# Performance work log

Measured on AMD Instinct MI355X. Metric: run time of the kernel, lower is better.

The kernel has to match this reference:

```python
import jax, jax.numpy as jnp
import numpy as np

HIDDEN = 128

def setup_inputs() -> dict:
    key = jax.random.key(0)
    k1, k2, k3, k4, k5, k6 = jax.random.split(key, 6)
    n_nodes, n_edges, h = 100000, 500000, HIDDEN
    node_features_after_gcn = jax.random.normal(k1, (n_nodes, h), dtype=jnp.float32)
    edges = jax.random.randint(k2, (2, n_edges), 0, n_nodes, dtype=jnp.int64)
    # edge_classifier params: Linear(2h -> 4h), Linear(4h -> 2)
    W1 = jax.random.normal(k3, (2 * h, 4 * h), dtype=jnp.float32) / np.sqrt(2 * h)
    b1 = jax.random.normal(k4, (4 * h,), dtype=jnp.float32) * 0.01
    W2 = jax.random.normal(k5, (4 * h, 2), dtype=jnp.float32) / np.sqrt(4 * h)
    b2 = jax.random.normal(k6, (2,), dtype=jnp.float32) * 0.01
    return {"node_features_after_gcn": node_features_after_gcn, "edges": edges,
            "W1": W1, "b1": b1, "W2": W2, "b2": b2}

def reference(node_features_after_gcn, W1, b1, W2, b2, edges):
    # gather endpoint features: [E, h] each (node1/node2 projections are Identity)
    first = node_features_after_gcn[edges[0], :]
    second = node_features_after_gcn[edges[1], :]
    edge_feat = jnp.concatenate((first, second), axis=1)  # [E, 2h]
    edge_feat = jax.nn.relu(edge_feat)
    hidden = jax.nn.relu(edge_feat @ W1 + b1)  # [E, 4h]
    return hidden @ W2 + b2  # [E, 2]
```

## Files before the change

kernel.cpp:

```cpp
#include <hip/hip_runtime.h>
#include <stdint.h>

#define HID  128
#define N1   512
#define NCAT 1024
#define NTB  48

typedef _Float16 f16;
typedef __attribute__((ext_vector_type(8))) _Float16 f16x8;
typedef __attribute__((ext_vector_type(4))) _Float16 f16x4;
typedef __attribute__((ext_vector_type(8))) short   short8;
typedef __attribute__((ext_vector_type(4))) float   floatx4;
typedef __attribute__((ext_vector_type(2))) float   floatx2;
typedef __attribute__((ext_vector_type(8))) __bf16  bf16x8;

static __device__ __forceinline__ short f2bf(float x) {
  uint32_t u = __builtin_bit_cast(uint32_t, x);
  uint32_t r = (u + 0x7FFFu + ((u >> 16) & 1u)) >> 16;
  return (short)r;
}
static __device__ __forceinline__ float bf2f(short s) {
  uint32_t u = ((uint32_t)(uint16_t)s) << 16;
  return __builtin_bit_cast(float, u);
}

static __device__ __forceinline__ void gload16(const f16* g, f16* l) {
  __builtin_amdgcn_global_load_lds(
      (const __attribute__((address_space(1))) unsigned int*)g,
      (__attribute__((address_space(3))) unsigned int*)l, 16, 0, 0);
}


__global__ __launch_bounds__(256) void prep_all(
    const float* __restrict__ feats, const float* __restrict__ W1,
    f16* __restrict__ A, f16* __restrict__ BT2, int total4) {
  int idx = blockIdx.x * 256 + threadIdx.x;
  if (idx < total4) {
    floatx4 f = *(const floatx4*)(feats + (size_t)idx * 4);
    f16x4 o;
#pragma unroll
    for (int j = 0; j < 4; ++j) o[j] = (f16)fmaxf(f[j], 0.f);
    *(f16x4*)(A + (size_t)idx * 4) = o;
    return;
  }
  int w = idx - total4;
  if (w < N1 * 256) {
    int n = w >> 8;
    int k = w & 255;
    BT2[w] = (f16)W1[k * N1 + n];
  }
}

__global__ __launch_bounds__(512, 2) void fused_kernel(
    const f16* __restrict__ A,
    const f16* __restrict__ BT2,
    const float* __restrict__ b1,
    const float* __restrict__ W2,
    const float* __restrict__ b2,
    const int* __restrict__ edges,
    float* __restrict__ out,
    int n_edges, int ntiles) {
  __shared__ f16 AU[2][NTB][HID];
  __shared__ f16 AV[2][NTB][HID];
  __shared__ float   part[8][NTB][2];
  __shared__ float   b1s[N1];
  __shared__ floatx2 w2s[N1];

  const int tid  = threadIdx.x;
  const int wave = tid >> 6;
  const int lane = tid & 63;
  const int quad = lane >> 4;
  const int l16  = lane & 15;
  const int n0w  = wave << 6;

  if (tid < N1) {
    b1s[tid] = b1[tid];
    w2s[tid] = *(const floatx2*)(W2 + 2 * tid);
  }

  f16x8 bfr[4][8];
#pragma unroll
  for (int nn = 0; nn < 4; ++nn) {
    const f16* bp = BT2 + (size_t)(n0w + nn * 16 + l16) * 256 + quad * 8;
#pragma unroll
    for (int kk = 0; kk < 8; ++kk) bfr[nn][kk] = *(const f16x8*)(bp + kk * 32);
  }

  const int j0   = wave * 3;
  const int rsub = lane >> 4;

  int idr[3];
  auto load_idx = [&](int t) {
#pragma unroll
    for (int c = 0; c < 3; ++c) {
      int j = j0 + c;
      int side = (j >= 12) ? 1 : 0;
      int r = ((j - side * 12) << 2) + rsub;
      int e = t * NTB + r;
      if (e >= n_edges) e = n_edges - 1;
      idr[c] = edges[side * n_edges + e];
    }
  };
  auto issue_gather = [&](int bb) {
#pragma unroll
    for (int c = 0; c < 3; ++c) {
      int j = j0 + c;
      int side = (j >= 12) ? 1 : 0;
      int r0 = (j - side * 12) << 2;
      int r  = r0 + rsub;
      const f16* src = A + ((size_t)idr[c] << 7) + (((lane & 15) ^ (r & 15)) << 3);
      f16* dst = side ? &AV[bb][r0][0] : &AU[bb][r0][0];
      gload16(src, dst);
    }
  };

  const int NB = gridDim.x;
  const int t0 = blockIdx.x;
  if (t0 < ntiles) {
    load_idx(t0);
    issue_gather(0);
    load_idx(t0 + NB);
  }

  int bb = 0;
  for (int t = t0; t < ntiles; t += NB) {
    __syncthreads();

    if (t + NB < ntiles) {
      issue_gather(bb ^ 1);
      load_idx(t + 2 * NB);
    }

    floatx4 acc[3][4];
#pragma unroll
    for (int mt = 0; mt < 3; ++mt)
#pragma unroll
      for (int nn = 0; nn < 4; ++nn) acc[mt][nn] = (floatx4){0.f, 0.f, 0.f, 0.f};

    const f16* au = &AU[bb][0][0];
    const f16* av = &AV[bb][0][0];
#pragma unroll
    for (int kk = 0; kk < 8; ++kk) {
      const f16* base = (kk < 4) ? au : av;
      const int coff = (((((kk & 3) << 2) + quad)) ^ l16) << 3;
      f16x8 a0 = *(const f16x8*)(base + (0 * 16 + l16) * HID + coff);
      f16x8 a1 = *(const f16x8*)(base + (1 * 16 + l16) * HID + coff);
      f16x8 a2 = *(const f16x8*)(base + (2 * 16 + l16) * HID + coff);
#pragma unroll
      for (int nn = 0; nn < 4; ++nn) {
        acc[0][nn] = __builtin_amdgcn_mfma_f32_16x16x32_f16(bfr[nn][kk], a0, acc[0][nn], 0, 0, 0);
        acc[1][nn] = __builtin_amdgcn_mfma_f32_16x16x32_f16(bfr[nn][kk], a1, acc[1][nn], 0, 0, 0);
        acc[2][nn] = __builtin_amdgcn_mfma_f32_16x16x32_f16(bfr[nn][kk], a2, acc[2][nn], 0, 0, 0);
      }
    }

    float s0[3] = {0.f, 0.f, 0.f};
    float s1[3] = {0.f, 0.f, 0.f};
#pragma unroll
    for (int nn = 0; nn < 4; ++nn) {
      const int nb = n0w + nn * 16 + (quad << 2);
      const floatx4 bv = *(const floatx4*)&b1s[nb];
      const floatx2 wa = w2s[nb + 0];
      const floatx2 wb = w2s[nb + 1];
      const floatx2 wc = w2s[nb + 2];
      const floatx2 wd = w2s[nb + 3];
#pragma unroll
      for (int mt = 0; mt < 3; ++mt) {
        float p0 = fmaxf(acc[mt][nn][0] + bv[0], 0.f);
        float p1 = fmaxf(acc[mt][nn][1] + bv[1], 0.f);
        float p2 = fmaxf(acc[mt][nn][2] + bv[2], 0.f);
        float p3 = fmaxf(acc[mt][nn][3] + bv[3], 0.f);
        s0[mt] += p0 * wa[0] + p1 * wb[0] + p2 * wc[0] + p3 * wd[0];
        s1[mt] += p0 * wa[1] + p1 * wb[1] + p2 * wc[1] + p3 * wd[1];
      }
    }
#pragma unroll
    for (int mt = 0; mt < 3; ++mt) {
      float a0 = s0[mt] + __shfl_xor(s0[mt], 16);
      a0 += __shfl_xor(a0, 32);
      float a1 = s1[mt] + __shfl_xor(s1[mt], 16);
      a1 += __shfl_xor(a1, 32);
      if (quad == 0) {
        floatx2 o = {a0, a1};
        *(floatx2*)&part[wave][mt * 16 + l16][0] = o;
      }
    }
    __syncthreads();
    if (tid < 2 * NTB) {
      const int m  = tid >> 1;
      const int jj = tid & 1;
      float s = part[0][m][jj] + part[1][m][jj] + part[2][m][jj] + part[3][m][jj]
              + part[4][m][jj] + part[5][m][jj] + part[6][m][jj] + part[7][m][jj];
      const int e = t * NTB + m;
      if (e < n_edges) out[2 * (size_t)e + jj] = s + b2[jj];
    }
    bb ^= 1;
  }
}


__global__ __launch_bounds__(256) void conv_bt_bf(
    const float* __restrict__ W1, short* __restrict__ BT) {
  int idx = blockIdx.x * 256 + threadIdx.x;
  int n = idx >> 7;
  int k = idx & 127;
  float w = (n < N1) ? W1[k * N1 + n] : W1[(k + HID) * N1 + (n - N1)];
  BT[idx] = f2bf(w);
}

__global__ __launch_bounds__(256) void gemm_bf(
    const float* __restrict__ feats, const short* __restrict__ BT,
    short* __restrict__ GH, int n_nodes) {
  const int wave = threadIdx.x >> 6;
  const int lane = threadIdx.x & 63;
  const int quad = lane >> 4;
  const int l16  = lane & 15;
  const int row0 = blockIdx.x * 64 + wave * 16;
  const int n0   = blockIdx.y * 128;
  const int m  = row0 + l16;
  const int mc = (m < n_nodes) ? m : (n_nodes - 1);
  const float* arow = feats + (size_t)mc * HID;
  floatx4 acc[8];
#pragma unroll
  for (int i = 0; i < 8; ++i) acc[i] = (floatx4){0.f, 0.f, 0.f, 0.f};
#pragma unroll
  for (int kk = 0; kk < 4; ++kk) {
    const int kbase = kk * 32 + quad * 8;
    floatx4 a0 = *(const floatx4*)(arow + kbase);
    floatx4 a1 = *(const floatx4*)(arow + kbase + 4);
    short8 af;
#pragma unroll
    for (int j = 0; j < 4; ++j) { float x = a0[j]; af[j] = f2bf(x > 0.f ? x : 0.f); }
#pragma unroll
    for (int j = 0; j < 4; ++j) { float x = a1[j]; af[4 + j] = f2bf(x > 0.f ? x : 0.f); }
    bf16x8 afrag = __builtin_bit_cast(bf16x8, af);
#pragma unroll
    for (int nn = 0; nn < 8; ++nn) {
      const int n = n0 + nn * 16 + l16;
      short8 bs = *(const short8*)(BT + (size_t)n * HID + kbase);
      acc[nn] = __builtin_amdgcn_mfma_f32_16x16x32_bf16(
          afrag, __builtin_bit_cast(bf16x8, bs), acc[nn], 0, 0, 0);
    }
  }
#pragma unroll
  for (int nn = 0; nn < 8; ++nn) {
    const int col = n0 + nn * 16 + l16;
#pragma unroll
    for (int r = 0; r < 4; ++r) {
      const int row = row0 + quad * 4 + r;
      if (row < n_nodes) GH[(size_t)row * NCAT + col] = f2bf(acc[nn][r]);
    }
  }
}

__global__ __launch_bounds__(256) void edge2_bf(
    const short* __restrict__ GH, const int* __restrict__ edges,
    const float* __restrict__ b1, const float* __restrict__ W2,
    const float* __restrict__ b2, float* __restrict__ out, int n_edges) {
  const int wave = threadIdx.x >> 6;
  const int lane = threadIdx.x & 63;
  const int w = blockIdx.x * 4 + wave;
  const int e0 = 2 * w;
  if (e0 >= n_edges) return;
  const bool has1 = (e0 + 1 < n_edges);
  const int j0 = lane * 8;
  const int u0 = edges[e0];
  const int v0 = edges[n_edges + e0];
  const int u1 = has1 ? edges[e0 + 1] : u0;
  const int v1 = has1 ? edges[n_edges + e0 + 1] : v0;
  short8 g0 = *(const short8*)(GH + (size_t)u0 * NCAT + j0);
  short8 h0 = *(const short8*)(GH + (size_t)v0 * NCAT + N1 + j0);
  short8 g1 = *(const short8*)(GH + (size_t)u1 * NCAT + j0);
  short8 h1 = *(const short8*)(GH + (size_t)v1 * NCAT + N1 + j0);
  float bv[8];
  {
    floatx4 t0 = *(const floatx4*)(b1 + j0);
    floatx4 t1 = *(const floatx4*)(b1 + j0 + 4);
#pragma unroll
    for (int j = 0; j < 4; ++j) { bv[j] = t0[j]; bv[4 + j] = t1[j]; }
  }
  float wv[16];
#pragma unroll
  for (int q = 0; q < 4; ++q) {
    floatx4 tt = *(const floatx4*)(W2 + (size_t)j0 * 2 + q * 4);
#pragma unroll
    for (int j = 0; j < 4; ++j) wv[q * 4 + j] = tt[j];
  }
  float s00 = 0.f, s01 = 0.f, s10 = 0.f, s11 = 0.f;
#pragma unroll
  for (int j = 0; j < 8; ++j) {
    float p0 = bf2f(g0[j]) + bf2f(h0[j]) + bv[j];
    p0 = p0 > 0.f ? p0 : 0.f;
    s00 += p0 * wv[2 * j];
    s01 += p0 * wv[2 * j + 1];
    float p1 = bf2f(g1[j]) + bf2f(h1[j]) + bv[j];
    p1 = p1 > 0.f ? p1 : 0.f;
    s10 += p1 * wv[2 * j];
    s11 += p1 * wv[2 * j + 1];
  }
#pragma unroll
  for (int off = 32; off > 0; off >>= 1) {
    s00 += __shfl_down(s00, off, 64);
    s01 += __shfl_down(s01, off, 64);
    s10 += __shfl_down(s10, off, 64);
    s11 += __shfl_down(s11, off, 64);
  }
  if (lane == 0) {
    out[2 * (size_t)e0]     = s00 + b2[0];
    out[2 * (size_t)e0 + 1] = s01 + b2[1];
    if (has1) {
      out[2 * (size_t)e0 + 2] = s10 + b2[0];
      out[2 * (size_t)e0 + 3] = s11 + b2[1];
    }
  }
}

__global__ __launch_bounds__(256) void slow_kernel(
    const float* __restrict__ feats, const int* __restrict__ edges,
    const float* __restrict__ W1, const float* __restrict__ b1,
    const float* __restrict__ W2, const float* __restrict__ b2,
    float* __restrict__ out, int n_edges) {
  const int wave = threadIdx.x >> 6;
  const int lane = threadIdx.x & 63;
  const int edge = blockIdx.x * 4 + wave;
  if (edge >= n_edges) return;
  const int u = edges[edge];
  const int v = edges[n_edges + edge];
  float f[4];
  f[0] = feats[(size_t)u * HID + lane];
  f[1] = feats[(size_t)u * HID + 64 + lane];
  f[2] = feats[(size_t)v * HID + lane];
  f[3] = feats[(size_t)v * HID + 64 + lane];
#pragma unroll
  for (int i = 0; i < 4; ++i) f[i] = f[i] > 0.f ? f[i] : 0.f;
  const int j0 = lane * 8;
  float acc[8];
#pragma unroll
  for (int j = 0; j < 8; ++j) acc[j] = 0.f;
#pragma unroll
  for (int seg = 0; seg < 4; ++seg) {
    float fs = f[seg];
    for (int k2 = 0; k2 < 64; ++k2) {
      float fk = __shfl(fs, k2, 64);
      const float* wr = W1 + (size_t)(seg * 64 + k2) * N1 + j0;
#pragma unroll
      for (int j = 0; j < 8; ++j) acc[j] += fk * wr[j];
    }
  }
  float s0 = 0.f, s1 = 0.f;
#pragma unroll
  for (int j = 0; j < 8; ++j) {
    float p = acc[j] + b1[j0 + j];
    p = p > 0.f ? p : 0.f;
    s0 += p * W2[(size_t)(j0 + j) * 2];
    s1 += p * W2[(size_t)(j0 + j) * 2 + 1];
  }
#pragma unroll
  for (int off = 32; off > 0; off >>= 1) {
    s0 += __shfl_down(s0, off, 64);
    s1 += __shfl_down(s1, off, 64);
  }
  if (lane == 0) {
    out[2 * (size_t)edge]     = s0 + b2[0];
    out[2 * (size_t)edge + 1] = s1 + b2[1];
  }
}

extern "C" void kernel_launch(void* const* d_in, const int* in_sizes, int n_in,
                              void* d_out, int out_size, void* d_ws, size_t ws_size,
                              hipStream_t stream) {
  const float* feats = (const float*)d_in[0];
  const int*   edges = (const int*)d_in[1];
  const float* W1    = (const float*)d_in[2];
  const float* b1    = (const float*)d_in[3];
  const float* W2    = (const float*)d_in[4];
  const float* b2    = (const float*)d_in[5];
  float* out = (float*)d_out;

  const int n_nodes = in_sizes[0] / HID;
  const int n_edges = in_sizes[1] / 2;

  const size_t bt2_bytes = (size_t)N1 * 256 * 2;
  const size_t a_bytes   = (size_t)n_nodes * HID * 2;

  const size_t bt_bytes = (size_t)NCAT * HID * 2;
  const size_t gh_bytes = (size_t)n_nodes * NCAT * 2;

  if (ws_size >= bt2_bytes + a_bytes) {
    f16* BT2 = (f16*)d_ws;
    f16* A   = (f16*)((char*)d_ws + bt2_bytes);
    const int total4 = n_nodes * (HID / 4);
    const int prep_total = total4 + N1 * 256;
    prep_all<<<(prep_total + 255) / 256, 256, 0, stream>>>(feats, W1, A, BT2, total4);
    const int ntiles = (n_edges + NTB - 1) / NTB;
    const int nb = ntiles < 256 ? ntiles : 256;
    fused_kernel<<<nb, 512, 0, stream>>>(A, BT2, b1, W2, b2, edges, out, n_edges, ntiles);
  } else if (ws_size >= bt_bytes + gh_bytes) {
    short* BT = (short*)d_ws;
    short* GH = (short*)((char*)d_ws + bt_bytes);
    conv_bt_bf<<<(NCAT * HID) / 256, 256, 0, stream>>>(W1, BT);
    dim3 grid((n_nodes + 63) / 64, NCAT / 128);
    gemm_bf<<<grid, 256, 0, stream>>>(feats, BT, GH, n_nodes);
    edge2_bf<<<((n_edges + 1) / 2 + 3) / 4, 256, 0, stream>>>(GH, edges, b1, W2, b2, out, n_edges);
  } else {
    slow_kernel<<<(n_edges + 3) / 4, 256, 0, stream>>>(feats, edges, W1, b1, W2, b2, out, n_edges);
  }
}
```

Measured before the change: 224.0 us.

## Fuse prep and edge MLP into one cooperative kernel with grid sync

Merges the feature/weight conversion kernel and the fused edge MLP kernel into a single cooperative launch. Each block first converts a grid-strided slice of features to relu'd fp16 and transposes W1, then waits at a grid-wide barrier before running the MFMA edge pipeline. This removes one kernel launch and the gap between the two kernels. The cost is that the prep phase now runs on only 256 blocks with 8-deep batched loads, and the grid sync adds latency. The old two-kernel path is kept as a fallback if the cooperative launch fails.

Result: slower. 340.4 us (+52.0%).

```diff
diff --git a/kernel.cpp b/kernel.cpp
--- a/kernel.cpp
+++ b/kernel.cpp
@@ -1,5 +1,8 @@
 #include <hip/hip_runtime.h>
+#include <hip/hip_cooperative_groups.h>
 #include <stdint.h>
+
+namespace cg = cooperative_groups;
 
 #define HID  128
 #define N1   512
@@ -9,6 +12,7 @@
 typedef _Float16 f16;
 typedef __attribute__((ext_vector_type(8))) _Float16 f16x8;
 typedef __attribute__((ext_vector_type(4))) _Float16 f16x4;
+typedef __attribute__((ext_vector_type(2))) _Float16 f16x2;
 typedef __attribute__((ext_vector_type(8))) short   short8;
 typedef __attribute__((ext_vector_type(4))) float   floatx4;
 typedef __attribute__((ext_vector_type(2))) float   floatx2;
@@ -23,6 +27,9 @@
   uint32_t u = ((uint32_t)(uint16_t)s) << 16;
   return __builtin_bit_cast(float, u);
 }
+static __device__ __forceinline__ f16x2 pkrtz(float a, float b) {
+  return __builtin_bit_cast(f16x2, __builtin_amdgcn_cvt_pkrtz(a, b));
+}
 
 static __device__ __forceinline__ void gload16(const f16* g, f16* l) {
   __builtin_amdgcn_global_load_lds(
@@ -31,35 +38,40 @@
 }
 
 
-__global__ __launch_bounds__(256) void prep_all(
+__global__ __launch_bounds__(512, 2) void mega_kernel(
     const float* __restrict__ feats, const float* __restrict__ W1,
-    f16* __restrict__ A, f16* __restrict__ BT2, int total4) {
-  int idx = blockIdx.x * 256 + threadIdx.x;
-  if (idx < total4) {
-    floatx4 f = *(const floatx4*)(feats + (size_t)idx * 4);
-    f16x4 o;
-#pragma unroll
-    for (int j = 0; j < 4; ++j) o[j] = (f16)fmaxf(f[j], 0.f);
-    *(f16x4*)(A + (size_t)idx * 4) = o;
-    return;
-  }
-  int w = idx - total4;
-  if (w < N1 * 256) {
-    int n = w >> 8;
-    int k = w & 255;
-    BT2[w] = (f16)W1[k * N1 + n];
-  }
-}
-
-__global__ __launch_bounds__(512, 2) void fused_kernel(
-    const f16* __restrict__ A,
-    const f16* __restrict__ BT2,
-    const float* __restrict__ b1,
-    const float* __restrict__ W2,
-    const float* __restrict__ b2,
-    const int* __restrict__ edges,
-    float* __restrict__ out,
-    int n_edges, int ntiles) {
+    f16* __restrict__ A, f16* __restrict__ BT2,
+    const float* __restrict__ b1, const float* __restrict__ W2,
+    const float* __restrict__ b2, const int* __restrict__ edges,
+    float* __restrict__ out, int n_edges, int ntiles, int total4) {
+  {
+    const int g  = blockIdx.x * 512 + threadIdx.x;
+    const int GS = gridDim.x * 512;
+    for (int base = g; base < total4; base += GS * 8) {
+      floatx4 v[8];
+#pragma unroll
+      for (int k = 0; k < 8; ++k) {
+        int u = base + k * GS;
+        if (u < total4) v[k] = *(const floatx4*)(feats + (size_t)u * 4);
+      }
+#pragma unroll
+      for (int k = 0; k < 8; ++k) {
+        int u = base + k * GS;
+        if (u < total4) {
+          f16x4 o;
+#pragma unroll
+          for (int j = 0; j < 4; ++j) o[j] = (f16)fmaxf(v[k][j], 0.f);
+          *(f16x4*)(A + (size_t)u * 4) = o;
+        }
+      }
+    }
+    for (int w = g; w < N1 * 256; w += GS) {
+      int n = w >> 8, k = w & 255;
+      BT2[w] = (f16)W1[k * N1 + n];
+    }
+  }
+  cg::this_grid().sync();
+
   __shared__ f16 AU[2][NTB][HID];
   __shared__ f16 AV[2][NTB][HID];
   __shared__ float   part[8][NTB][2];
@@ -77,6 +89,7 @@
     b1s[tid] = b1[tid];
     w2s[tid] = *(const floatx2*)(W2 + 2 * tid);
   }
+  const float b2v0 = b2[0], b2v1 = b2[1];
 
   f16x8 bfr[4][8];
 #pragma unroll
@@ -101,15 +114,15 @@
       idr[c] = edges[side * n_edges + e];
     }
   };
-  auto issue_gather = [&](int bb) {
+  auto issue_gather = [&](int b) {
 #pragma unroll
     for (int c = 0; c < 3; ++c) {
       int j = j0 + c;
       int side = (j >= 12) ? 1 : 0;
       int r0 = (j - side * 12) << 2;
       int r  = r0 + rsub;
-      const f16* src = A + ((size_t)idr[c] << 7) + (((lane & 15) ^ (r & 15)) << 3);
-      f16* dst = side ? &AV[bb][r0][0] : &AU[bb][r0][0];
+      const f16* src = A + ((size_t)idr[c] << 7) + ((l16 ^ (r & 15)) << 3);
+      f16* dst = side ? &AV[b][r0][0] : &AU[b][r0][0];
       gload16(src, dst);
     }
   };
@@ -180,10 +193,8 @@
       a0 += __shfl_xor(a0, 32);
       float a1 = s1[mt] + __shfl_xor(s1[mt], 16);
       a1 += __shfl_xor(a1, 32);
-      if (quad == 0) {
-        floatx2 o = {a0, a1};
-        *(floatx2*)&part[wave][mt * 16 + l16][0] = o;
-      }
+      if (quad == 0)
+        *(floatx2*)&part[wave][mt * 16 + l16][0] = (floatx2){a0, a1};
     }
     __syncthreads();
     if (tid < 2 * NTB) {
@@ -192,7 +203,170 @@
       float s = part[0][m][jj] + part[1][m][jj] + part[2][m][jj] + part[3][m][jj]
               + part[4][m][jj] + part[5][m][jj] + part[6][m][jj] + part[7][m][jj];
       const int e = t * NTB + m;
-      if (e < n_edges) out[2 * (size_t)e + jj] = s + b2[jj];
+      if (e < n_edges) out[2 * (size_t)e + jj] = s + (jj ? b2v1 : b2v0);
+    }
+    bb ^= 1;
+  }
+}
+
+
+__global__ __launch_bounds__(256) void prep_all(
+    const float* __restrict__ feats, const float* __restrict__ W1,
+    f16* __restrict__ A, f16* __restrict__ BT2, int total4) {
+  int idx = blockIdx.x * 256 + threadIdx.x;
+  if (idx < total4) {
+    floatx4 f = *(const floatx4*)(feats + (size_t)idx * 4);
+    f16x4 o;
+#pragma unroll
+    for (int j = 0; j < 4; ++j) o[j] = (f16)fmaxf(f[j], 0.f);
+    *(f16x4*)(A + (size_t)idx * 4) = o;
+    return;
+  }
+  int w = idx - total4;
+  if (w < N1 * 256) {
+    int n = w >> 8;
+    int k = w & 255;
+    BT2[w] = (f16)W1[k * N1 + n];
+  }
+}
+
+__global__ __launch_bounds__(512, 2) void fused_kernel(
+    const f16* __restrict__ A, const f16* __restrict__ BT2,
+    const float* __restrict__ b1, const float* __restrict__ W2,
+    const float* __restrict__ b2, const int* __restrict__ edges,
+    float* __restrict__ out, int n_edges, int ntiles) {
+  __shared__ f16 AU[2][NTB][HID];
+  __shared__ f16 AV[2][NTB][HID];
+  __shared__ float   part[8][NTB][2];
+  __shared__ float   b1s[N1];
+  __shared__ floatx2 w2s[N1];
+
+  const int tid  = threadIdx.x;
+  const int wave = tid >> 6;
+  const int lane = tid & 63;
+  const int quad = lane >> 4;
+  const int l16  = lane & 15;
+  const int n0w  = wave << 6;
+
+  if (tid < N1) {
+    b1s[tid] = b1[tid];
+    w2s[tid] = *(const floatx2*)(W2 + 2 * tid);
+  }
+  const float b2v0 = b2[0], b2v1 = b2[1];
+
+  f16x8 bfr[4][8];
+#pragma unroll
+  for (int nn = 0; nn < 4; ++nn) {
+    const f16* bp = BT2 + (size_t)(n0w + nn * 16 + l16) * 256 + quad * 8;
+#pragma unroll
+    for (int kk = 0; kk < 8; ++kk) bfr[nn][kk] = *(const f16x8*)(bp + kk * 32);
+  }
+
+  const int j0   = wave * 3;
+  const int rsub = lane >> 4;
+
+  int idr[3];
+  auto load_idx = [&](int t) {
+#pragma unroll
+    for (int c = 0; c < 3; ++c) {
+      int j = j0 + c;
+      int side = (j >= 12) ? 1 : 0;
+      int r = ((j - side * 12) << 2) + rsub;
+      int e = t * NTB + r;
+      if (e >= n_edges) e = n_edges - 1;
+      idr[c] = edges[side * n_edges + e];
+    }
+  };
+  auto issue_gather = [&](int b) {
+#pragma unroll
+    for (int c = 0; c < 3; ++c) {
+      int j = j0 + c;
+      int side = (j >= 12) ? 1 : 0;
+      int r0 = (j - side * 12) << 2;
+      int r  = r0 + rsub;
+      const f16* src = A + ((size_t)idr[c] << 7) + ((l16 ^ (r & 15)) << 3);
+      f16* dst = side ? &AV[b][r0][0] : &AU[b][r0][0];
+      gload16(src, dst);
+    }
+  };
+
+  const int NB = gridDim.x;
+  const int t0 = blockIdx.x;
+  if (t0 < ntiles) {
+    load_idx(t0);
+    issue_gather(0);
+    load_idx(t0 + NB);
+  }
+
+  int bb = 0;
+  for (int t = t0; t < ntiles; t += NB) {
+    __syncthreads();
+
+    if (t + NB < ntiles) {
+      issue_gather(bb ^ 1);
+      load_idx(t + 2 * NB);
+    }
+
+    floatx4 acc[3][4];
+#pragma unroll
+    for (int mt = 0; mt < 3; ++mt)
+#pragma unroll
+      for (int nn = 0; nn < 4; ++nn) acc[mt][nn] = (floatx4){0.f, 0.f, 0.f, 0.f};
+
+    const f16* au = &AU[bb][0][0];
+    const f16* av = &AV[bb][0][0];
+#pragma unroll
+    for (int kk = 0; kk < 8; ++kk) {
+      const f16* base = (kk < 4) ? au : av;
+      const int coff = (((((kk & 3) << 2) + quad)) ^ l16) << 3;
+      f16x8 a0 = *(const f16x8*)(base + (0 * 16 + l16) * HID + coff);
+      f16x8 a1 = *(const f16x8*)(base + (1 * 16 + l16) * HID + coff);
+      f16x8 a2 = *(const f16x8*)(base + (2 * 16 + l16) * HID + coff);
+#pragma unroll
+      for (int nn = 0; nn < 4; ++nn) {
+        acc[0][nn] = __builtin_amdgcn_mfma_f32_16x16x32_f16(bfr[nn][kk], a0, acc[0][nn], 0, 0, 0);
+        acc[1][nn] = __builtin_amdgcn_mfma_f32_16x16x32_f16(bfr[nn][kk], a1, acc[1][nn], 0, 0, 0);
+        acc[2][nn] = __builtin_amdgcn_mfma_f32_16x16x32_f16(bfr[nn][kk], a2, acc[2][nn], 0, 0, 0);
+      }
+    }
+
+    float s0[3] = {0.f, 0.f, 0.f};
+    float s1[3] = {0.f, 0.f, 0.f};
+#pragma unroll
+    for (int nn = 0; nn < 4; ++nn) {
+      const int nb = n0w + nn * 16 + (quad << 2);
+      const floatx4 bv = *(const floatx4*)&b1s[nb];
+      const floatx2 wa = w2s[nb + 0];
+      const floatx2 wb = w2s[nb + 1];
+      const floatx2 wc = w2s[nb + 2];
+      const floatx2 wd = w2s[nb + 3];
+#pragma unroll
+      for (int mt = 0; mt < 3; ++mt) {
+        float p0 = fmaxf(acc[mt][nn][0] + bv[0], 0.f);
+        float p1 = fmaxf(acc[mt][nn][1] + bv[1], 0.f);
+        float p2 = fmaxf(acc[mt][nn][2] + bv[2], 0.f);
+        float p3 = fmaxf(acc[mt][nn][3] + bv[3], 0.f);
+        s0[mt] += p0 * wa[0] + p1 * wb[0] + p2 * wc[0] + p3 * wd[0];
+        s1[mt] += p0 * wa[1] + p1 * wb[1] + p2 * wc[1] + p3 * wd[1];
+      }
+    }
+#pragma unroll
+    for (int mt = 0; mt < 3; ++mt) {
+      float a0 = s0[mt] + __shfl_xor(s0[mt], 16);
+      a0 += __shfl_xor(a0, 32);
+      float a1 = s1[mt] + __shfl_xor(s1[mt], 16);
+      a1 += __shfl_xor(a1, 32);
+      if (quad == 0)
+        *(floatx2*)&part[wave][mt * 16 + l16][0] = (floatx2){a0, a1};
+    }
+    __syncthreads();
+    if (tid < 2 * NTB) {
+      const int m  = tid >> 1;
+      const int jj = tid & 1;
+      float s = part[0][m][jj] + part[1][m][jj] + part[2][m][jj] + part[3][m][jj]
+              + part[4][m][jj] + part[5][m][jj] + part[6][m][jj] + part[7][m][jj];
+      const int e = t * NTB + m;
+      if (e < n_edges) out[2 * (size_t)e + jj] = s + (jj ? b2v1 : b2v0);
     }
     bb ^= 1;
   }
@@ -389,12 +563,20 @@
   if (ws_size >= bt2_bytes + a_bytes) {
     f16* BT2 = (f16*)d_ws;
     f16* A   = (f16*)((char*)d_ws + bt2_bytes);
-    const int total4 = n_nodes * (HID / 4);
-    const int prep_total = total4 + N1 * 256;
-    prep_all<<<(prep_total + 255) / 256, 256, 0, stream>>>(feats, W1, A, BT2, total4);
-    const int ntiles = (n_edges + NTB - 1) / NTB;
-    const int nb = ntiles < 256 ? ntiles : 256;
-    fused_kernel<<<nb, 512, 0, stream>>>(A, BT2, b1, W2, b2, edges, out, n_edges, ntiles);
+    int total4 = n_nodes * (HID / 4);
+    int ntiles = (n_edges + NTB - 1) / NTB;
+    int nb = ntiles < 256 ? ntiles : 256;
+
+    void* args[] = {(void*)&feats, (void*)&W1, (void*)&A, (void*)&BT2,
+                    (void*)&b1, (void*)&W2, (void*)&b2, (void*)&edges,
+                    (void*)&out, (void*)&n_edges, (void*)&ntiles, (void*)&total4};
+    hipError_t err = hipLaunchCooperativeKernel(
+        (const void*)mega_kernel, dim3(nb), dim3(512), args, 0, stream);
+    if (err != hipSuccess) {
+      const int prep_total = total4 + N1 * 256;
+      prep_all<<<(prep_total + 255) / 256, 256, 0, stream>>>(feats, W1, A, BT2, total4);
+      fused_kernel<<<nb, 512, 0, stream>>>(A, BT2, b1, W2, b2, edges, out, n_edges, ntiles);
+    }
   } else if (ws_size >= bt_bytes + gh_bytes) {
     short* BT = (short*)d_ws;
     short* GH = (short*)((char*)d_ws + bt_bytes);
```

## Split hidden dimension across block pairs and combine outputs with atomics

Applied to the files above, without the earlier changes.

Each edge tile is now processed by two blocks, each covering half of the 512 hidden columns, which halves the per-wave B-fragment registers and raises launch bounds to 4 blocks per CU. Partial results from the two halves are combined with float atomicAdd into an output zeroed during the prep kernel, and only one half adds b2. This trades duplicated gathers of edge features (each tile's A rows are loaded twice) and atomic traffic for higher occupancy and more blocks in flight.

After: 339.9 us. 51.7% more time.

```diff
diff --git a/kernel.cpp b/kernel.cpp
--- a/kernel.cpp
+++ b/kernel.cpp
@@ -9,6 +9,7 @@
 typedef _Float16 f16;
 typedef __attribute__((ext_vector_type(8))) _Float16 f16x8;
 typedef __attribute__((ext_vector_type(4))) _Float16 f16x4;
+typedef __attribute__((ext_vector_type(2))) _Float16 f16x2;
 typedef __attribute__((ext_vector_type(8))) short   short8;
 typedef __attribute__((ext_vector_type(4))) float   floatx4;
 typedef __attribute__((ext_vector_type(2))) float   floatx2;
@@ -33,7 +34,8 @@
 
 __global__ __launch_bounds__(256) void prep_all(
     const float* __restrict__ feats, const float* __restrict__ W1,
-    f16* __restrict__ A, f16* __restrict__ BT2, int total4) {
+    f16* __restrict__ A, f16* __restrict__ BT2,
+    float* __restrict__ out, int total4, int nout) {
   int idx = blockIdx.x * 256 + threadIdx.x;
   if (idx < total4) {
     floatx4 f = *(const floatx4*)(feats + (size_t)idx * 4);
@@ -48,10 +50,13 @@
     int n = w >> 8;
     int k = w & 255;
     BT2[w] = (f16)W1[k * N1 + n];
-  }
-}
-
-__global__ __launch_bounds__(512, 2) void fused_kernel(
+    return;
+  }
+  int w2 = w - N1 * 256;
+  if (w2 < nout) out[w2] = 0.f;
+}
+
+__global__ __launch_bounds__(512, 4) void fused_kernel(
     const f16* __restrict__ A,
     const f16* __restrict__ BT2,
     const float* __restrict__ b1,
@@ -71,16 +76,19 @@
   const int lane = tid & 63;
   const int quad = lane >> 4;
   const int l16  = lane & 15;
-  const int n0w  = wave << 6;
+  const int colh = blockIdx.x & 1;
+  const int n0w  = (colh << 8) | (wave << 5);
 
   if (tid < N1) {
     b1s[tid] = b1[tid];
     w2s[tid] = *(const floatx2*)(W2 + 2 * tid);
   }
-
-  f16x8 bfr[4][8];
-#pragma unroll
-  for (int nn = 0; nn < 4; ++nn) {
+  const float b2v0 = colh ? 0.f : b2[0];
+  const float b2v1 = colh ? 0.f : b2[1];
+
+  f16x8 bfr[2][8];
+#pragma unroll
+  for (int nn = 0; nn < 2; ++nn) {
     const f16* bp = BT2 + (size_t)(n0w + nn * 16 + l16) * 256 + quad * 8;
 #pragma unroll
     for (int kk = 0; kk < 8; ++kk) bfr[nn][kk] = *(const f16x8*)(bp + kk * 32);
@@ -101,41 +109,42 @@
       idr[c] = edges[side * n_edges + e];
     }
   };
-  auto issue_gather = [&](int bb) {
+  auto issue_gather = [&](int b) {
 #pragma unroll
     for (int c = 0; c < 3; ++c) {
       int j = j0 + c;
       int side = (j >= 12) ? 1 : 0;
       int r0 = (j - side * 12) << 2;
       int r  = r0 + rsub;
-      const f16* src = A + ((size_t)idr[c] << 7) + (((lane & 15) ^ (r & 15)) << 3);
-      f16* dst = side ? &AV[bb][r0][0] : &AU[bb][r0][0];
+      const f16* src = A + ((size_t)idr[c] << 7) + ((l16 ^ (r & 15)) << 3);
+      f16* dst = side ? &AV[b][r0][0] : &AU[b][r0][0];
       gload16(src, dst);
     }
   };
 
-  const int NB = gridDim.x;
-  const int t0 = blockIdx.x;
+  const int NBT = gridDim.x >> 1;
+  const int t0  = blockIdx.x >> 1;
   if (t0 < ntiles) {
     load_idx(t0);
     issue_gather(0);
-    load_idx(t0 + NB);
+    load_idx(t0 + NBT);
   }
 
   int bb = 0;
-  for (int t = t0; t < ntiles; t += NB) {
+  for (int t = t0; t < ntiles; t += NBT) {
     __syncthreads();
 
-    if (t + NB < ntiles) {
+    if (t + NBT < ntiles) {
       issue_gather(bb ^ 1);
-      load_idx(t + 2 * NB);
-    }
-
-    floatx4 acc[3][4];
-#pragma unroll
-    for (int mt = 0; mt < 3; ++mt)
-#pragma unroll
-      for (int nn = 0; nn < 4; ++nn) acc[mt][nn] = (floatx4){0.f, 0.f, 0.f, 0.f};
+      load_idx(t + 2 * NBT);
+    }
+
+    floatx4 acc[3][2];
+#pragma unroll
+    for (int mt = 0; mt < 3; ++mt) {
+      acc[mt][0] = (floatx4){0.f, 0.f, 0.f, 0.f};
+      acc[mt][1] = (floatx4){0.f, 0.f, 0.f, 0.f};
+    }
 
     const f16* au = &AU[bb][0][0];
     const f16* av = &AV[bb][0][0];
@@ -147,7 +156,7 @@
       f16x8 a1 = *(const f16x8*)(base + (1 * 16 + l16) * HID + coff);
       f16x8 a2 = *(const f16x8*)(base + (2 * 16 + l16) * HID + coff);
 #pragma unroll
-      for (int nn = 0; nn < 4; ++nn) {
+      for (int nn = 0; nn < 2; ++nn) {
         acc[0][nn] = __builtin_amdgcn_mfma_f32_16x16x32_f16(bfr[nn][kk], a0, acc[0][nn], 0, 0, 0);
         acc[1][nn] = __builtin_amdgcn_mfma_f32_16x16x32_f16(bfr[nn][kk], a1, acc[1][nn], 0, 0, 0);
         acc[2][nn] = __builtin_amdgcn_mfma_f32_16x16x32_f16(bfr[nn][kk], a2, acc[2][nn], 0, 0, 0);
@@ -157,7 +166,7 @@
     float s0[3] = {0.f, 0.f, 0.f};
     float s1[3] = {0.f, 0.f, 0.f};
 #pragma unroll
-    for (int nn = 0; nn < 4; ++nn) {
+    for (int nn = 0; nn < 2; ++nn) {
       const int nb = n0w + nn * 16 + (quad << 2);
       const floatx4 bv = *(const floatx4*)&b1s[nb];
       const floatx2 wa = w2s[nb + 0];
@@ -180,10 +189,8 @@
       a0 += __shfl_xor(a0, 32);
       float a1 = s1[mt] + __shfl_xor(s1[mt], 16);
       a1 += __shfl_xor(a1, 32);
-      if (quad == 0) {
-        floatx2 o = {a0, a1};
-        *(floatx2*)&part[wave][mt * 16 + l16][0] = o;
-      }
+      if (quad == 0)
+        *(floatx2*)&part[wave][mt * 16 + l16][0] = (floatx2){a0, a1};
     }
     __syncthreads();
     if (tid < 2 * NTB) {
@@ -192,7 +199,8 @@
       float s = part[0][m][jj] + part[1][m][jj] + part[2][m][jj] + part[3][m][jj]
               + part[4][m][jj] + part[5][m][jj] + part[6][m][jj] + part[7][m][jj];
       const int e = t * NTB + m;
-      if (e < n_edges) out[2 * (size_t)e + jj] = s + b2[jj];
+      if (e < n_edges)
+        atomicAdd(out + 2 * (size_t)e + jj, s + (jj ? b2v1 : b2v0));
     }
     bb ^= 1;
   }
@@ -390,11 +398,14 @@
     f16* BT2 = (f16*)d_ws;
     f16* A   = (f16*)((char*)d_ws + bt2_bytes);
     const int total4 = n_nodes * (HID / 4);
-    const int prep_total = total4 + N1 * 256;
-    prep_all<<<(prep_total + 255) / 256, 256, 0, stream>>>(feats, W1, A, BT2, total4);
+    const int nout = 2 * n_edges;
+    const int prep_total = total4 + N1 * 256 + nout;
+    prep_all<<<(prep_total + 255) / 256, 256, 0, stream>>>(
+        feats, W1, A, BT2, out, total4, nout);
     const int ntiles = (n_edges + NTB - 1) / NTB;
-    const int nb = ntiles < 256 ? ntiles : 256;
-    fused_kernel<<<nb, 512, 0, stream>>>(A, BT2, b1, W2, b2, edges, out, n_edges, ntiles);
+    int nbt = ntiles < 256 ? ntiles : 256;
+    fused_kernel<<<2 * nbt, 512, 0, stream>>>(A, BT2, b1, W2, b2, edges,
+                                              out, n_edges, ntiles);
   } else if (ws_size >= bt_bytes + gh_bytes) {
     short* BT = (short*)d_ws;
     short* GH = (short*)((char*)d_ws + bt_bytes);
```

## Interleave gather prefetch into MFMA k-loop with barriers and priority

Applied to the files above, without the earlier changes.

Spreads the next tile's global-to-LDS gathers and index loads across the first k-iterations of the MFMA loop instead of issuing them all before compute. Each k-step gets workgroup barriers, an lgkmcnt wait and raised wave priority around the MFMA block, in a ping-pong style schedule. b2 is also hoisted into registers. The extra per-iteration barriers (16 per tile) add sync overhead and may serialize waves more than the interleaving hides.

Measured after the change: 297.7 us. +32.9%, slower.

```diff
diff --git a/kernel.cpp b/kernel.cpp
--- a/kernel.cpp
+++ b/kernel.cpp
@@ -9,6 +9,7 @@
 typedef _Float16 f16;
 typedef __attribute__((ext_vector_type(8))) _Float16 f16x8;
 typedef __attribute__((ext_vector_type(4))) _Float16 f16x4;
+typedef __attribute__((ext_vector_type(2))) _Float16 f16x2;
 typedef __attribute__((ext_vector_type(8))) short   short8;
 typedef __attribute__((ext_vector_type(4))) float   floatx4;
 typedef __attribute__((ext_vector_type(2))) float   floatx2;
@@ -77,6 +78,7 @@
     b1s[tid] = b1[tid];
     w2s[tid] = *(const floatx2*)(W2 + 2 * tid);
   }
+  const float b2v0 = b2[0], b2v1 = b2[1];
 
   f16x8 bfr[4][8];
 #pragma unroll
@@ -101,24 +103,23 @@
       idr[c] = edges[side * n_edges + e];
     }
   };
-  auto issue_gather = [&](int bb) {
-#pragma unroll
-    for (int c = 0; c < 3; ++c) {
-      int j = j0 + c;
-      int side = (j >= 12) ? 1 : 0;
-      int r0 = (j - side * 12) << 2;
-      int r  = r0 + rsub;
-      const f16* src = A + ((size_t)idr[c] << 7) + (((lane & 15) ^ (r & 15)) << 3);
-      f16* dst = side ? &AV[bb][r0][0] : &AU[bb][r0][0];
-      gload16(src, dst);
-    }
+  auto issue_gather_one = [&](int b, int c) {
+    int j = j0 + c;
+    int side = (j >= 12) ? 1 : 0;
+    int r0 = (j - side * 12) << 2;
+    int r  = r0 + rsub;
+    const f16* src = A + ((size_t)idr[c] << 7) + ((l16 ^ (r & 15)) << 3);
+    f16* dst = side ? &AV[b][r0][0] : &AU[b][r0][0];
+    gload16(src, dst);
   };
 
   const int NB = gridDim.x;
   const int t0 = blockIdx.x;
   if (t0 < ntiles) {
     load_idx(t0);
-    issue_gather(0);
+    issue_gather_one(0, 0);
+    issue_gather_one(0, 1);
+    issue_gather_one(0, 2);
     load_idx(t0 + NB);
   }
 
@@ -126,10 +127,7 @@
   for (int t = t0; t < ntiles; t += NB) {
     __syncthreads();
 
-    if (t + NB < ntiles) {
-      issue_gather(bb ^ 1);
-      load_idx(t + 2 * NB);
-    }
+    const bool doPf = (t + NB < ntiles);
 
     floatx4 acc[3][4];
 #pragma unroll
@@ -146,12 +144,22 @@
       f16x8 a0 = *(const f16x8*)(base + (0 * 16 + l16) * HID + coff);
       f16x8 a1 = *(const f16x8*)(base + (1 * 16 + l16) * HID + coff);
       f16x8 a2 = *(const f16x8*)(base + (2 * 16 + l16) * HID + coff);
+      if (doPf) {
+        if (kk < 3) issue_gather_one(bb ^ 1, kk);
+        else if (kk == 3) load_idx(t + 2 * NB);
+      }
+      __builtin_amdgcn_s_barrier();
+      asm volatile("s_waitcnt lgkmcnt(0)" ::: "memory");
+      __builtin_amdgcn_sched_barrier(0);
+      __builtin_amdgcn_s_setprio(1);
 #pragma unroll
       for (int nn = 0; nn < 4; ++nn) {
         acc[0][nn] = __builtin_amdgcn_mfma_f32_16x16x32_f16(bfr[nn][kk], a0, acc[0][nn], 0, 0, 0);
         acc[1][nn] = __builtin_amdgcn_mfma_f32_16x16x32_f16(bfr[nn][kk], a1, acc[1][nn], 0, 0, 0);
         acc[2][nn] = __builtin_amdgcn_mfma_f32_16x16x32_f16(bfr[nn][kk], a2, acc[2][nn], 0, 0, 0);
       }
+      __builtin_amdgcn_s_setprio(0);
+      __builtin_amdgcn_s_barrier();
     }
 
     float s0[3] = {0.f, 0.f, 0.f};
@@ -180,10 +188,8 @@
       a0 += __shfl_xor(a0, 32);
       float a1 = s1[mt] + __shfl_xor(s1[mt], 16);
       a1 += __shfl_xor(a1, 32);
-      if (quad == 0) {
-        floatx2 o = {a0, a1};
-        *(floatx2*)&part[wave][mt * 16 + l16][0] = o;
-      }
+      if (quad == 0)
+        *(floatx2*)&part[wave][mt * 16 + l16][0] = (floatx2){a0, a1};
     }
     __syncthreads();
     if (tid < 2 * NTB) {
@@ -192,7 +198,7 @@
       float s = part[0][m][jj] + part[1][m][jj] + part[2][m][jj] + part[3][m][jj]
               + part[4][m][jj] + part[5][m][jj] + part[6][m][jj] + part[7][m][jj];
       const int e = t * NTB + m;
-      if (e < n_edges) out[2 * (size_t)e + jj] = s + b2[jj];
+      if (e < n_edges) out[2 * (size_t)e + jj] = s + (jj ? b2v1 : b2v0);
     }
     bb ^= 1;
   }
```
